# Optimization experiments

Hardware: AMD Instinct MI355X
Metric: run time of the kernel (lower is better)

The kernel has to match this reference:

```python
import math
import jax, jax.numpy as jnp
import numpy as np

B, T, C, H = 2, 4096, 512, 8  # batch, seq_len, n_embd, n_head
D = C // H                    # head_dim = 64

def setup_inputs() -> dict:
    key = jax.random.key(0)
    k1, k2, k3 = jax.random.split(key, 3)
    x = jax.random.normal(k1, (B, T, C), dtype=jnp.float32)
    # torch Linear(C, 3C, bias=False): y = x @ W.T; we store the transposed
    # weight directly so the forward is x @ W_attn.
    W_attn = jax.random.normal(k2, (C, 3 * C), dtype=jnp.float32) * 0.02
    W_proj = jax.random.normal(k3, (C, C), dtype=jnp.float32) * 0.02
    return {"x": x, "W_attn": W_attn, "W_proj": W_proj}

def reference(x, W_attn, W_proj):
    b, t, c = x.shape
    # fused QKV projection, split like .split(n_embd, dim=2)
    qkv = x @ W_attn                              # [B,T,3C]
    q, k, v = jnp.split(qkv, 3, axis=-1)          # each [B,T,C]
    def to_heads(u):
        return u.reshape(b, t, H, D).transpose(0, 2, 1, 3)  # [B,H,T,D]
    q, k, v = to_heads(q), to_heads(k), to_heads(v)
    scale = 1.0 / math.sqrt(D)
    att = jnp.einsum('bhqd,bhkd->bhqk', q, k) * scale       # [B,H,T,T]
    causal = jnp.tril(jnp.ones((t, t), dtype=bool))         # masked_fill(triu(...,1), -inf)
    att = jnp.where(causal, att, -jnp.inf)
    probs = jax.nn.softmax(att, axis=-1)
    y = jnp.einsum('bhqk,bhkd->bhqd', probs, v)             # [B,H,T,D]
    y = y.transpose(0, 2, 1, 3).reshape(b, t, c)            # [B,T,C]
    return y @ W_proj
```

## Files before the change

### kernel.cpp

```cpp
#include <hip/hip_runtime.h>
#include <hip/hip_bf16.h>
#include <stdint.h>


typedef __attribute__((ext_vector_type(8))) short short8;
typedef __attribute__((ext_vector_type(4))) float floatx4;
typedef __attribute__((ext_vector_type(16))) float floatx16;
#if __has_builtin(__builtin_amdgcn_permlane32_swap)
typedef __attribute__((ext_vector_type(2))) unsigned int uint2v;
#define HAVE_PLSWAP 1
#else
#define HAVE_PLSWAP 0
#endif

__device__ __forceinline__ unsigned short f2bf(float f) {
    unsigned int x = __float_as_uint(f);
    unsigned int r = x + 0x7fffu + ((x >> 16) & 1u);
    return (unsigned short)(r >> 16);
}

__device__ __forceinline__ unsigned int pk_bf16(float a, float b) {
    __hip_bfloat162 p = __float22bfloat162_rn(make_float2(a, b));
    return *reinterpret_cast<unsigned int*>(&p);
}

__device__ __forceinline__ float bfsum2(unsigned int w) {
    return __uint_as_float(w << 16) + __uint_as_float(w & 0xffff0000u);
}

__global__ __launch_bounds__(256) void prep_a(
    const float* __restrict__ x, unsigned short* __restrict__ xb,
    const float* __restrict__ Wa, unsigned short* __restrict__ WaT)
{
    const int bid = blockIdx.x;
    const int tid = threadIdx.x;
    if (bid < 2048) {
        size_t i = ((size_t)bid * 256 + tid) * 8;
        float4 a = *reinterpret_cast<const float4*>(x + i);
        float4 b = *reinterpret_cast<const float4*>(x + i + 4);
        unsigned short o[8] = {f2bf(a.x), f2bf(a.y), f2bf(a.z), f2bf(a.w),
                               f2bf(b.x), f2bf(b.y), f2bf(b.z), f2bf(b.w)};
        *reinterpret_cast<uint4*>(xb + i) = *reinterpret_cast<uint4*>(o);
    } else {
        __shared__ unsigned short tile[32][34];
        const int t2 = bid - 2048;
        const int n0 = (t2 % 48) * 32, k0 = (t2 / 48) * 32;
        const int tx = tid & 31, ty = tid >> 5;
        #pragma unroll
        for (int p = 0; p < 4; ++p)
            tile[tx][ty + p * 8] = f2bf(Wa[(size_t)(k0 + ty + p * 8) * 1536 + n0 + tx]);
        __syncthreads();
        #pragma unroll
        for (int p = 0; p < 4; ++p)
            WaT[(size_t)(n0 + ty + p * 8) * 512 + k0 + tx] = tile[ty + p * 8][tx];
    }
}

__global__ __launch_bounds__(256) void transpose_wp(
    const float* __restrict__ W, unsigned short* __restrict__ Wt)
{
    __shared__ unsigned short tile[32][34];
    const int tid = threadIdx.x;
    const int tx = tid & 31, ty = tid >> 5;
    const int n0 = blockIdx.x * 32, k0 = blockIdx.y * 32;
    #pragma unroll
    for (int p = 0; p < 4; ++p)
        tile[tx][ty + p * 8] = f2bf(W[(size_t)(k0 + ty + p * 8) * 512 + n0 + tx]);
    __syncthreads();
    #pragma unroll
    for (int p = 0; p < 4; ++p)
        Wt[(size_t)(n0 + ty + p * 8) * 512 + k0 + tx] = tile[ty + p * 8][tx];
}

template<int EPI>
__global__ __launch_bounds__(256) void mm_bt(
    const unsigned short* __restrict__ A,
    const unsigned short* __restrict__ Bt,
    void* __restrict__ outp)
{
    __shared__ __align__(16) unsigned char smem[40960];

    const int tid  = threadIdx.x;
    const int wave = tid >> 6;
    const int lane = tid & 63;
    const int quad = lane >> 4;
    const int l16  = lane & 15;
    const int wr   = wave >> 1;
    const int wc   = wave & 1;
    const int m0 = blockIdx.x * 128;
    const int n0 = blockIdx.y * 128;

    floatx4 acc[4][4];
    #pragma unroll
    for (int i = 0; i < 4; ++i)
        #pragma unroll
        for (int j = 0; j < 4; ++j) acc[i][j] = (floatx4){0.f, 0.f, 0.f, 0.f};

    const int row = tid >> 1;
    const int cb  = (tid & 1) * 16;

    const unsigned short* ap = &A[(size_t)(m0 + row) * 512 + cb];
    const unsigned short* bp = &Bt[(size_t)(n0 + row) * 512 + cb];

    uint4 ra0 = *reinterpret_cast<const uint4*>(ap);
    uint4 ra1 = *reinterpret_cast<const uint4*>(ap + 8);
    uint4 rb0 = *reinterpret_cast<const uint4*>(bp);
    uint4 rb1 = *reinterpret_cast<const uint4*>(bp + 8);
    {
        auto Al = reinterpret_cast<unsigned short(*)[40]>(smem);
        auto Bl = reinterpret_cast<unsigned short(*)[40]>(smem + 10240);
        *reinterpret_cast<uint4*>(&Al[row][cb])     = ra0;
        *reinterpret_cast<uint4*>(&Al[row][cb + 8]) = ra1;
        *reinterpret_cast<uint4*>(&Bl[row][cb])     = rb0;
        *reinterpret_cast<uint4*>(&Bl[row][cb + 8]) = rb1;
    }

    for (int it = 0; it < 16; ++it) {
        __syncthreads();
        const int k0 = it * 32;
        if (it < 15) {
            ra0 = *reinterpret_cast<const uint4*>(ap + k0 + 32);
            ra1 = *reinterpret_cast<const uint4*>(ap + k0 + 40);
            rb0 = *reinterpret_cast<const uint4*>(bp + k0 + 32);
            rb1 = *reinterpret_cast<const uint4*>(bp + k0 + 40);
        }

        auto Al = reinterpret_cast<unsigned short(*)[40]>(smem + (it & 1) * 20480);
        auto Bl = reinterpret_cast<unsigned short(*)[40]>(smem + (it & 1) * 20480 + 10240);

        short8 af[4], bf[4];
        #pragma unroll
        for (int ti = 0; ti < 4; ++ti)
            af[ti] = *reinterpret_cast<const short8*>(&Al[wr * 64 + ti * 16 + l16][quad * 8]);
        #pragma unroll
        for (int tj = 0; tj < 4; ++tj)
            bf[tj] = *reinterpret_cast<const short8*>(&Bl[wc * 64 + tj * 16 + l16][quad * 8]);
        #pragma unroll
        for (int ti = 0; ti < 4; ++ti)
            #pragma unroll
            for (int tj = 0; tj < 4; ++tj)
                acc[ti][tj] = __builtin_amdgcn_mfma_f32_16x16x32_bf16(af[ti], bf[tj], acc[ti][tj], 0, 0, 0);

        if (it < 15) {
            auto An = reinterpret_cast<unsigned short(*)[40]>(smem + ((it + 1) & 1) * 20480);
            auto Bn = reinterpret_cast<unsigned short(*)[40]>(smem + ((it + 1) & 1) * 20480 + 10240);
            *reinterpret_cast<uint4*>(&An[row][cb])     = ra0;
            *reinterpret_cast<uint4*>(&An[row][cb + 8]) = ra1;
            *reinterpret_cast<uint4*>(&Bn[row][cb])     = rb0;
            *reinterpret_cast<uint4*>(&Bn[row][cb + 8]) = rb1;
        }
    }

    if (EPI == 0) {
        unsigned short* WS = (unsigned short*)outp;
        unsigned short* Qb  = WS;
        unsigned short* Kb  = WS + 4194304;
        unsigned short* Vtb = WS + 8388608;
        const int which = n0 >> 9;
        const int h = ((n0 + wc * 64) >> 6) & 7;

        if (which == 2) {
            auto Tr = reinterpret_cast<unsigned short(*)[80]>(smem);
            __syncthreads();
            #pragma unroll
            for (int ti = 0; ti < 4; ++ti)
                #pragma unroll
                for (int tj = 0; tj < 4; ++tj) {
                    unsigned int lo = pk_bf16(acc[ti][tj][0], acc[ti][tj][1]);
                    unsigned int hi = pk_bf16(acc[ti][tj][2], acc[ti][tj][3]);
                    *reinterpret_cast<uint2*>(&Tr[(wave << 6) + tj * 16 + l16][ti * 16 + quad * 4])
                        = make_uint2(lo, hi);
                }
            const int b = m0 >> 12;
            const int bh = b * 8 + h;
            const int t0g = (m0 & 4095) + wr * 64;
            const int tseg = (lane & 7) * 8;
            #pragma unroll
            for (int p = 0; p < 8; ++p) {
                int dl = p * 8 + (lane >> 3);
                uint4 v = *reinterpret_cast<const uint4*>(&Tr[(wave << 6) + dl][tseg]);
                *reinterpret_cast<uint4*>(&Vtb[((size_t)(bh * 64 + dl)) * 4096 + t0g + tseg]) = v;
            }
        } else {
            const float sc = (which == 0) ? 0.18033688f : 1.0f;
            #pragma unroll
            for (int ti = 0; ti < 4; ++ti) {
                #pragma unroll
                for (int r = 0; r < 4; ++r) {
                    int m = m0 + wr * 64 + ti * 16 + quad * 4 + r;
                    int b = m >> 12, t = m & 4095;
                    int bh = b * 8 + h;
                    #pragma unroll
                    for (int tj = 0; tj < 4; ++tj) {
                        int d = tj * 16 + l16;
                        unsigned short val = f2bf(acc[ti][tj][r] * sc);
                        if (which == 0) Qb[((size_t)bh * 4096 + t) * 64 + d] = val;
                        else            Kb[((size_t)bh * 4096 + t) * 64 + d] = val;
                    }
                }
            }
        }
    } else {
        float* Out = (float*)outp;
        #pragma unroll
        for (int ti = 0; ti < 4; ++ti) {
            #pragma unroll
            for (int r = 0; r < 4; ++r) {
                int m = m0 + wr * 64 + ti * 16 + quad * 4 + r;
                #pragma unroll
                for (int tj = 0; tj < 4; ++tj) {
                    int n = n0 + wc * 64 + tj * 16 + l16;
                    Out[(size_t)m * 512 + n] = acc[ti][tj][r];
                }
            }
        }
    }
}

__global__ __launch_bounds__(256) void attn_mfma(
    const unsigned short* __restrict__ Q,
    const unsigned short* __restrict__ K,
    const unsigned short* __restrict__ Vt,
    unsigned short* __restrict__ Y)
{
    __shared__ __align__(16) unsigned short Kc[2][64][64];
    __shared__ __align__(16) unsigned short Vc[2][64][64];
    __shared__ __align__(16) float Ws[4][32];

    const int tid  = threadIdx.x;
    const int wave = tid >> 6;
    const int lane = tid & 63;
    const int l32  = lane & 31;
    const int hh   = lane >> 5;
    const int sw7  = lane & 7;

    const int bid = blockIdx.x;
    const int bh  = bid & 15;
    const int u   = (bid >> 4) & 15;
    const int ilo = (bid >> 8) ? (31 - u) : u;
    const int ihi = 63 - ilo;
    const int qbw = (wave < 2) ? ilo : ihi;
    const int qg0 = qbw * 64 + (wave & 1) * 32;

    const unsigned short* Qp = Q  + (size_t)bh * (4096 * 64);
    const unsigned short* Kp = K  + (size_t)bh * (4096 * 64);
    const unsigned short* Vp = Vt + (size_t)bh * (64 * 4096);

    short8 qf[4];
    #pragma unroll
    for (int k16 = 0; k16 < 4; ++k16)
        qf[k16] = *reinterpret_cast<const short8*>(
            &Qp[(size_t)(qg0 + l32) * 64 + k16 * 16 + hh * 8]);

    floatx16 o0 = {0,0,0,0,0,0,0,0,0,0,0,0,0,0,0,0};
    floatx16 o1 = {0,0,0,0,0,0,0,0,0,0,0,0,0,0,0,0};
    float rs = 0.f;

    const int rr  = tid >> 3;
    const int cc  = tid & 7;
    const int c0  = cc * 8;
    const int scs = ((cc ^ (rr & 7)) << 3);

    uint4 rk0 = *reinterpret_cast<const uint4*>(&Kp[(size_t)rr * 64 + c0]);
    uint4 rk1 = *reinterpret_cast<const uint4*>(&Kp[(size_t)(rr + 32) * 64 + c0]);
    uint4 rv0 = *reinterpret_cast<const uint4*>(&Vp[(size_t)rr * 4096 + c0]);
    uint4 rv1 = *reinterpret_cast<const uint4*>(&Vp[(size_t)(rr + 32) * 4096 + c0]);
    *reinterpret_cast<uint4*>(&Kc[0][rr][scs])      = rk0;
    *reinterpret_cast<uint4*>(&Kc[0][rr + 32][scs]) = rk1;
    *reinterpret_cast<uint4*>(&Vc[0][rr][scs])      = rv0;
    *reinterpret_cast<uint4*>(&Vc[0][rr + 32][scs]) = rv1;

    const int NT = ihi + 1;
    for (int kt = 0; kt < NT; ++kt) {
        __syncthreads();
        const int cur = kt & 1;
        const int nxt = cur ^ 1;

        if (kt + 1 < NT) {
            const int jn = (kt + 1) * 64;
            rk0 = *reinterpret_cast<const uint4*>(&Kp[(size_t)(jn + rr) * 64 + c0]);
            rk1 = *reinterpret_cast<const uint4*>(&Kp[(size_t)(jn + rr + 32) * 64 + c0]);
            rv0 = *reinterpret_cast<const uint4*>(&Vp[(size_t)rr * 4096 + jn + c0]);
            rv1 = *reinterpret_cast<const uint4*>(&Vp[(size_t)(rr + 32) * 4096 + jn + c0]);
        }

        if (kt <= qbw) {
            floatx16 s0 = {0,0,0,0,0,0,0,0,0,0,0,0,0,0,0,0};
            floatx16 s1 = {0,0,0,0,0,0,0,0,0,0,0,0,0,0,0,0};
            #pragma unroll
            for (int k16 = 0; k16 < 4; ++k16) {
                const int chs = ((k16 * 2 + hh) ^ sw7) << 3;
                short8 a0 = *reinterpret_cast<const short8*>(&Kc[cur][l32][chs]);
                short8 a1 = *reinterpret_cast<const short8*>(&Kc[cur][32 + l32][chs]);
                s0 = __builtin_amdgcn_mfma_f32_32x32x16_bf16(a0, qf[k16], s0, 0, 0, 0);
                s1 = __builtin_amdgcn_mfma_f32_32x32x16_bf16(a1, qf[k16], s1, 0, 0, 0);
            }
            if (kt == qbw) {
                const int ql = (wave & 1) * 32 + l32;
                #pragma unroll
                for (int r = 0; r < 16; ++r) {
                    const int kl = (r & 3) + 8 * (r >> 2) + 4 * hh;
                    s0[r] = (kl      <= ql) ? s0[r] : -1e30f;
                    s1[r] = (kl + 32 <= ql) ? s1[r] : -1e30f;
                }
            }
            #pragma unroll
            for (int r = 0; r < 16; ++r) {
                s0[r] = __builtin_amdgcn_exp2f(s0[r]);
                s1[r] = __builtin_amdgcn_exp2f(s1[r]);
            }

            short8 pa[4];
            #pragma unroll
            for (int t = 0; t < 2; ++t) {
                float e0  = t ? s1[0]  : s0[0],  e1  = t ? s1[1]  : s0[1];
                float e2  = t ? s1[2]  : s0[2],  e3  = t ? s1[3]  : s0[3];
                float e4  = t ? s1[4]  : s0[4],  e5  = t ? s1[5]  : s0[5];
                float e6  = t ? s1[6]  : s0[6],  e7  = t ? s1[7]  : s0[7];
                float e8  = t ? s1[8]  : s0[8],  e9  = t ? s1[9]  : s0[9];
                float e10 = t ? s1[10] : s0[10], e11 = t ? s1[11] : s0[11];
                float e12 = t ? s1[12] : s0[12], e13 = t ? s1[13] : s0[13];
                float e14 = t ? s1[14] : s0[14], e15 = t ? s1[15] : s0[15];
                unsigned int A0 = pk_bf16(e0, e1),   B0 = pk_bf16(e2, e3);
                unsigned int A1 = pk_bf16(e4, e5),   B1 = pk_bf16(e6, e7);
                unsigned int A2 = pk_bf16(e8, e9),   B2 = pk_bf16(e10, e11);
                unsigned int A3 = pk_bf16(e12, e13), B3 = pk_bf16(e14, e15);
                rs += bfsum2(A0) + bfsum2(B0) + bfsum2(A1) + bfsum2(B1)
                    + bfsum2(A2) + bfsum2(B2) + bfsum2(A3) + bfsum2(B3);
#if HAVE_PLSWAP
                uint2v rA = __builtin_amdgcn_permlane32_swap(A0, A1, false, false);
                uint2v rB = __builtin_amdgcn_permlane32_swap(B0, B1, false, false);
                uint4 u0 = make_uint4(rA[0], rB[0], rA[1], rB[1]);
                pa[t * 2] = *reinterpret_cast<short8*>(&u0);
                rA = __builtin_amdgcn_permlane32_swap(A2, A3, false, false);
                rB = __builtin_amdgcn_permlane32_swap(B2, B3, false, false);
                uint4 u1 = make_uint4(rA[0], rB[0], rA[1], rB[1]);
                pa[t * 2 + 1] = *reinterpret_cast<short8*>(&u1);
#else
                unsigned int pA0 = __shfl_xor((int)A0, 32), pA1 = __shfl_xor((int)A1, 32);
                unsigned int pB0 = __shfl_xor((int)B0, 32), pB1 = __shfl_xor((int)B1, 32);
                unsigned int pA2 = __shfl_xor((int)A2, 32), pA3 = __shfl_xor((int)A3, 32);
                unsigned int pB2 = __shfl_xor((int)B2, 32), pB3 = __shfl_xor((int)B3, 32);
                uint4 u0 = make_uint4(hh ? pA1 : A0, hh ? pB1 : B0,
                                      hh ? A1 : pA0, hh ? B1 : pB0);
                pa[t * 2] = *reinterpret_cast<short8*>(&u0);
                uint4 u1 = make_uint4(hh ? pA3 : A2, hh ? pB3 : B2,
                                      hh ? A3 : pA2, hh ? B3 : pB2);
                pa[t * 2 + 1] = *reinterpret_cast<short8*>(&u1);
#endif
            }

            #pragma unroll
            for (int f = 0; f < 4; ++f) {
                const int chs = ((f * 2 + hh) ^ sw7) << 3;
                short8 b0 = *reinterpret_cast<const short8*>(&Vc[cur][l32][chs]);
                short8 b1 = *reinterpret_cast<const short8*>(&Vc[cur][32 + l32][chs]);
                o0 = __builtin_amdgcn_mfma_f32_32x32x16_bf16(pa[f], b0, o0, 0, 0, 0);
                o1 = __builtin_amdgcn_mfma_f32_32x32x16_bf16(pa[f], b1, o1, 0, 0, 0);
            }
        }

        if (kt + 1 < NT) {
            *reinterpret_cast<uint4*>(&Kc[nxt][rr][scs])      = rk0;
            *reinterpret_cast<uint4*>(&Kc[nxt][rr + 32][scs]) = rk1;
            *reinterpret_cast<uint4*>(&Vc[nxt][rr][scs])      = rv0;
            *reinterpret_cast<uint4*>(&Vc[nxt][rr + 32][scs]) = rv1;
        }
    }

    float tot = rs + __shfl_xor(rs, 32);
    if (lane < 32) Ws[wave][l32] = 1.0f / tot;
    __syncthreads();

    float4 iv[4];
    #pragma unroll
    for (int g = 0; g < 4; ++g)
        iv[g] = *reinterpret_cast<const float4*>(&Ws[wave][g * 8 + hh * 4]);

    const int b = bh >> 3, h = bh & 7;
    #pragma unroll
    for (int g = 0; g < 4; ++g) {
        #pragma unroll
        for (int rsub = 0; rsub < 4; ++rsub) {
            const int r = g * 4 + rsub;
            const int t = qg0 + 8 * g + 4 * hh + rsub;
            const float sc = iv[g][rsub];
            unsigned short* yr = &Y[((size_t)(b * 4096 + t)) * 512 + h * 64];
            yr[l32]      = f2bf(o0[r] * sc);
            yr[32 + l32] = f2bf(o1[r] * sc);
        }
    }
}

extern "C" void kernel_launch(void* const* d_in, const int* in_sizes, int n_in,
                              void* d_out, int out_size, void* d_ws, size_t ws_size,
                              hipStream_t stream) {
    const float* x  = (const float*)d_in[0];
    const float* Wa = (const float*)d_in[1];
    const float* Wp = (const float*)d_in[2];
    float* out = (float*)d_out;
    unsigned short* ws = (unsigned short*)d_ws;

    unsigned short* Qb  = ws;
    unsigned short* Kb  = ws + 4194304;
    unsigned short* Vtb = ws + 8388608;
    unsigned short* Yb  = ws + 12582912;
    unsigned short* WaT = Yb;
    unsigned short* WpT = Qb;
    unsigned short* xb  = (unsigned short*)d_out;

    prep_a<<<dim3(2816), dim3(256), 0, stream>>>(x, xb, Wa, WaT);
    mm_bt<0><<<dim3(64, 12), dim3(256), 0, stream>>>(xb, WaT, (void*)ws);
    attn_mfma<<<dim3(512), dim3(256), 0, stream>>>(Qb, Kb, Vtb, Yb);
    transpose_wp<<<dim3(16, 16), dim3(256), 0, stream>>>(Wp, WpT);
    mm_bt<1><<<dim3(64, 4), dim3(256), 0, stream>>>(Yb, WpT, (void*)out);
}
```

Measured before the change: 187.8 us.

## Split attention key tiles across wave pairs and reduce partial outputs in LDS

Each block now handles a single 64-row query block instead of a paired low/high block, and the grid doubles to 1024 blocks. Within a block, two waves share the same 32 query rows and each takes half of every 64-key tile, so each wave does one score MFMA chain instead of two. The partial outputs and row sums are combined through LDS reused from the K/V buffers at the end. The goal is more parallelism and shorter per-wave dependency chains, at the cost of an extra LDS reduction and less even causal load balance per block.

After: 165.7 us. -11.8%, faster.

```diff
diff --git a/kernel.cpp b/kernel.cpp
--- a/kernel.cpp
+++ b/kernel.cpp
@@ -225,22 +225,22 @@
 {
     __shared__ __align__(16) unsigned short Kc[2][64][64];
     __shared__ __align__(16) unsigned short Vc[2][64][64];
-    __shared__ __align__(16) float Ws[4][32];
 
     const int tid  = threadIdx.x;
     const int wave = tid >> 6;
     const int lane = tid & 63;
     const int l32  = lane & 31;
     const int hh   = lane >> 5;
-    const int sw7  = lane & 7;
+    const int swz  = l32 & 7;
+    const int p    = wave >> 1;
+    const int w    = wave & 1;
 
     const int bid = blockIdx.x;
     const int bh  = bid & 15;
-    const int u   = (bid >> 4) & 15;
-    const int ilo = (bid >> 8) ? (31 - u) : u;
-    const int ihi = 63 - ilo;
-    const int qbw = (wave < 2) ? ilo : ihi;
-    const int qg0 = qbw * 64 + (wave & 1) * 32;
+    const int j   = (bid >> 4) & 15;
+    const int g   = bid >> 8;
+    const int qb  = (g == 0) ? j : (g == 1) ? (63 - j) : (g == 2) ? (16 + j) : (47 - j);
+    const int m0  = qb * 64;
 
     const unsigned short* Qp = Q  + (size_t)bh * (4096 * 64);
     const unsigned short* Kp = K  + (size_t)bh * (4096 * 64);
@@ -250,7 +250,7 @@
     #pragma unroll
     for (int k16 = 0; k16 < 4; ++k16)
         qf[k16] = *reinterpret_cast<const short8*>(
-            &Qp[(size_t)(qg0 + l32) * 64 + k16 * 16 + hh * 8]);
+            &Qp[(size_t)(m0 + 32 * p + l32) * 64 + k16 * 16 + hh * 8]);
 
     floatx16 o0 = {0,0,0,0,0,0,0,0,0,0,0,0,0,0,0,0};
     floatx16 o1 = {0,0,0,0,0,0,0,0,0,0,0,0,0,0,0,0};
@@ -270,7 +270,7 @@
     *reinterpret_cast<uint4*>(&Vc[0][rr][scs])      = rv0;
     *reinterpret_cast<uint4*>(&Vc[0][rr + 32][scs]) = rv1;
 
-    const int NT = ihi + 1;
+    const int NT = qb + 1;
     for (int kt = 0; kt < NT; ++kt) {
         __syncthreads();
         const int cur = kt & 1;
@@ -284,75 +284,62 @@
             rv1 = *reinterpret_cast<const uint4*>(&Vp[(size_t)(rr + 32) * 4096 + jn + c0]);
         }
 
-        if (kt <= qbw) {
-            floatx16 s0 = {0,0,0,0,0,0,0,0,0,0,0,0,0,0,0,0};
-            floatx16 s1 = {0,0,0,0,0,0,0,0,0,0,0,0,0,0,0,0};
+        const bool active = (kt < qb) || (w == 0) || (p == 1);
+        if (active) {
+            floatx16 s = {0,0,0,0,0,0,0,0,0,0,0,0,0,0,0,0};
             #pragma unroll
             for (int k16 = 0; k16 < 4; ++k16) {
-                const int chs = ((k16 * 2 + hh) ^ sw7) << 3;
-                short8 a0 = *reinterpret_cast<const short8*>(&Kc[cur][l32][chs]);
-                short8 a1 = *reinterpret_cast<const short8*>(&Kc[cur][32 + l32][chs]);
-                s0 = __builtin_amdgcn_mfma_f32_32x32x16_bf16(a0, qf[k16], s0, 0, 0, 0);
-                s1 = __builtin_amdgcn_mfma_f32_32x32x16_bf16(a1, qf[k16], s1, 0, 0, 0);
-            }
-            if (kt == qbw) {
-                const int ql = (wave & 1) * 32 + l32;
+                const int chs = ((2 * k16 + hh) ^ swz) << 3;
+                short8 a = *reinterpret_cast<const short8*>(&Kc[cur][32 * w + l32][chs]);
+                s = __builtin_amdgcn_mfma_f32_32x32x16_bf16(a, qf[k16], s, 0, 0, 0);
+            }
+            if (kt == qb) {
+                const int ql = 32 * p + l32;
                 #pragma unroll
                 for (int r = 0; r < 16; ++r) {
-                    const int kl = (r & 3) + 8 * (r >> 2) + 4 * hh;
-                    s0[r] = (kl      <= ql) ? s0[r] : -1e30f;
-                    s1[r] = (kl + 32 <= ql) ? s1[r] : -1e30f;
+                    const int kl = 32 * w + (r & 3) + 8 * (r >> 2) + 4 * hh;
+                    s[r] = (kl <= ql) ? s[r] : -1e30f;
                 }
             }
             #pragma unroll
-            for (int r = 0; r < 16; ++r) {
-                s0[r] = __builtin_amdgcn_exp2f(s0[r]);
-                s1[r] = __builtin_amdgcn_exp2f(s1[r]);
-            }
-
-            short8 pa[4];
-            #pragma unroll
-            for (int t = 0; t < 2; ++t) {
-                float e0  = t ? s1[0]  : s0[0],  e1  = t ? s1[1]  : s0[1];
-                float e2  = t ? s1[2]  : s0[2],  e3  = t ? s1[3]  : s0[3];
-                float e4  = t ? s1[4]  : s0[4],  e5  = t ? s1[5]  : s0[5];
-                float e6  = t ? s1[6]  : s0[6],  e7  = t ? s1[7]  : s0[7];
-                float e8  = t ? s1[8]  : s0[8],  e9  = t ? s1[9]  : s0[9];
-                float e10 = t ? s1[10] : s0[10], e11 = t ? s1[11] : s0[11];
-                float e12 = t ? s1[12] : s0[12], e13 = t ? s1[13] : s0[13];
-                float e14 = t ? s1[14] : s0[14], e15 = t ? s1[15] : s0[15];
-                unsigned int A0 = pk_bf16(e0, e1),   B0 = pk_bf16(e2, e3);
-                unsigned int A1 = pk_bf16(e4, e5),   B1 = pk_bf16(e6, e7);
-                unsigned int A2 = pk_bf16(e8, e9),   B2 = pk_bf16(e10, e11);
-                unsigned int A3 = pk_bf16(e12, e13), B3 = pk_bf16(e14, e15);
-                rs += bfsum2(A0) + bfsum2(B0) + bfsum2(A1) + bfsum2(B1)
-                    + bfsum2(A2) + bfsum2(B2) + bfsum2(A3) + bfsum2(B3);
+            for (int r = 0; r < 16; ++r) s[r] = __builtin_amdgcn_exp2f(s[r]);
+
+            unsigned int A0 = pk_bf16(s[0],  s[1]),  B0 = pk_bf16(s[2],  s[3]);
+            unsigned int A1 = pk_bf16(s[4],  s[5]),  B1 = pk_bf16(s[6],  s[7]);
+            unsigned int A2 = pk_bf16(s[8],  s[9]),  B2 = pk_bf16(s[10], s[11]);
+            unsigned int A3 = pk_bf16(s[12], s[13]), B3 = pk_bf16(s[14], s[15]);
+            rs += bfsum2(A0) + bfsum2(B0) + bfsum2(A1) + bfsum2(B1)
+                + bfsum2(A2) + bfsum2(B2) + bfsum2(A3) + bfsum2(B3);
+            short8 pa[2];
 #if HAVE_PLSWAP
+            {
                 uint2v rA = __builtin_amdgcn_permlane32_swap(A0, A1, false, false);
                 uint2v rB = __builtin_amdgcn_permlane32_swap(B0, B1, false, false);
                 uint4 u0 = make_uint4(rA[0], rB[0], rA[1], rB[1]);
-                pa[t * 2] = *reinterpret_cast<short8*>(&u0);
+                pa[0] = *reinterpret_cast<short8*>(&u0);
                 rA = __builtin_amdgcn_permlane32_swap(A2, A3, false, false);
                 rB = __builtin_amdgcn_permlane32_swap(B2, B3, false, false);
                 uint4 u1 = make_uint4(rA[0], rB[0], rA[1], rB[1]);
-                pa[t * 2 + 1] = *reinterpret_cast<short8*>(&u1);
+                pa[1] = *reinterpret_cast<short8*>(&u1);
+            }
 #else
+            {
                 unsigned int pA0 = __shfl_xor((int)A0, 32), pA1 = __shfl_xor((int)A1, 32);
                 unsigned int pB0 = __shfl_xor((int)B0, 32), pB1 = __shfl_xor((int)B1, 32);
                 unsigned int pA2 = __shfl_xor((int)A2, 32), pA3 = __shfl_xor((int)A3, 32);
                 unsigned int pB2 = __shfl_xor((int)B2, 32), pB3 = __shfl_xor((int)B3, 32);
                 uint4 u0 = make_uint4(hh ? pA1 : A0, hh ? pB1 : B0,
                                       hh ? A1 : pA0, hh ? B1 : pB0);
-                pa[t * 2] = *reinterpret_cast<short8*>(&u0);
+                pa[0] = *reinterpret_cast<short8*>(&u0);
                 uint4 u1 = make_uint4(hh ? pA3 : A2, hh ? pB3 : B2,
                                       hh ? A3 : pA2, hh ? B3 : pB2);
-                pa[t * 2 + 1] = *reinterpret_cast<short8*>(&u1);
+                pa[1] = *reinterpret_cast<short8*>(&u1);
+            }
 #endif
-            }
-
-            #pragma unroll
-            for (int f = 0; f < 4; ++f) {
-                const int chs = ((f * 2 + hh) ^ sw7) << 3;
+
+            #pragma unroll
+            for (int f = 0; f < 2; ++f) {
+                const int chs = ((4 * w + 2 * f + hh) ^ swz) << 3;
                 short8 b0 = *reinterpret_cast<const short8*>(&Vc[cur][l32][chs]);
                 short8 b1 = *reinterpret_cast<const short8*>(&Vc[cur][32 + l32][chs]);
                 o0 = __builtin_amdgcn_mfma_f32_32x32x16_bf16(pa[f], b0, o0, 0, 0, 0);
@@ -368,26 +355,34 @@
         }
     }
 
+    __syncthreads();
+    float* Ob  = reinterpret_cast<float*>(&Kc[0][0][0]);
+    float* Wsf = reinterpret_cast<float*>(&Vc[0][0][0]);
     float tot = rs + __shfl_xor(rs, 32);
-    if (lane < 32) Ws[wave][l32] = 1.0f / tot;
+    if (lane < 32) Wsf[(p * 2 + w) * 32 + l32] = tot;
+    #pragma unroll
+    for (int r = 0; r < 16; ++r) {
+        const int qloc = (r & 3) + 8 * (r >> 2) + 4 * hh;
+        Ob[((p * 2 + w) * 32 + qloc) * 32 + l32] = w ? o0[r] : o1[r];
+    }
     __syncthreads();
 
-    float4 iv[4];
-    #pragma unroll
-    for (int g = 0; g < 4; ++g)
-        iv[g] = *reinterpret_cast<const float4*>(&Ws[wave][g * 8 + hh * 4]);
-
     const int b = bh >> 3, h = bh & 7;
     #pragma unroll
-    for (int g = 0; g < 4; ++g) {
+    for (int gg = 0; gg < 4; ++gg) {
+        float4 a4 = *reinterpret_cast<const float4*>(&Wsf[(p * 2 + 0) * 32 + 8 * gg + 4 * hh]);
+        float4 b4 = *reinterpret_cast<const float4*>(&Wsf[(p * 2 + 1) * 32 + 8 * gg + 4 * hh]);
+        const float ivv[4] = {1.f / (a4.x + b4.x), 1.f / (a4.y + b4.y),
+                              1.f / (a4.z + b4.z), 1.f / (a4.w + b4.w)};
         #pragma unroll
         for (int rsub = 0; rsub < 4; ++rsub) {
-            const int r = g * 4 + rsub;
-            const int t = qg0 + 8 * g + 4 * hh + rsub;
-            const float sc = iv[g][rsub];
-            unsigned short* yr = &Y[((size_t)(b * 4096 + t)) * 512 + h * 64];
-            yr[l32]      = f2bf(o0[r] * sc);
-            yr[32 + l32] = f2bf(o1[r] * sc);
+            const int r = gg * 4 + rsub;
+            const int qloc = 8 * gg + 4 * hh + rsub;
+            const float part = Ob[((p * 2 + (1 - w)) * 32 + qloc) * 32 + l32];
+            const float mine = w ? o1[r] : o0[r];
+            const int t = m0 + 32 * p + qloc;
+            Y[((size_t)(b * 4096 + t)) * 512 + h * 64 + 32 * w + l32]
+                = f2bf((mine + part) * ivv[rsub]);
         }
     }
 }
@@ -411,7 +406,7 @@
 
     prep_a<<<dim3(2816), dim3(256), 0, stream>>>(x, xb, Wa, WaT);
     mm_bt<0><<<dim3(64, 12), dim3(256), 0, stream>>>(xb, WaT, (void*)ws);
-    attn_mfma<<<dim3(512), dim3(256), 0, stream>>>(Qb, Kb, Vtb, Yb);
+    attn_mfma<<<dim3(1024), dim3(256), 0, stream>>>(Qb, Kb, Vtb, Yb);
     transpose_wp<<<dim3(16, 16), dim3(256), 0, stream>>>(Wp, WpT);
     mm_bt<1><<<dim3(64, 4), dim3(256), 0, stream>>>(Yb, WpT, (void*)out);
 }
```
